# Performance work log

Hardware: AMD Instinct MI355X
Metric: run time of the kernel (lower is better)

The kernel has to match this reference:

```python
import jax, jax.numpy as jnp
import numpy as np

D_MODEL = 4096
D_FF = 16384
BATCH = 1
SEQ = 1024


def setup_inputs() -> dict:
    key = jax.random.key(0)
    k_x, k_k, k_s = jax.random.split(key, 3)
    inputs = jax.random.normal(k_x, (BATCH, SEQ, D_MODEL), dtype=jnp.float32)
    # int4 quantized kernel, values in [-8, 8)
    kernel = jax.random.randint(k_k, (D_MODEL, D_FF), -8, 8, dtype=jnp.int32).astype(jnp.int4)
    # per-output-channel scale, shape (1, D_FF), strictly positive
    scale = jax.random.uniform(k_s, (1, D_FF), dtype=jnp.float32, minval=0.5, maxval=2.0)
    return {"inputs": inputs, "kernel": kernel, "scale": scale}


def reference(inputs, kernel, scale):
    # Dequantize: int4 kernel -> fp32, divide by per-channel scale
    kernel_f = kernel.astype(jnp.float32) / scale  # [D_MODEL, D_FF]
    # btd,df->btf
    return jnp.einsum("btd,df->btf", inputs, kernel_f)
```

## Files before the change

kernel.cpp:

```cpp
#include <hip/hip_runtime.h>
#include <hip/hip_bf16.h>

#define D_MODEL 4096
#define D_FF    16384
#define SEQ     1024

typedef __attribute__((ext_vector_type(4))) float          fvec4;
typedef __attribute__((ext_vector_type(4))) float          f32x4;
typedef __attribute__((ext_vector_type(4))) int            i32x4;
typedef __attribute__((ext_vector_type(8))) short          bf16x8;
typedef __attribute__((ext_vector_type(4))) unsigned short u16x4;

constexpr int BM = 256, BN = 256, BK = 64;
constexpr int NTHREADS = 512;
constexpr int NT = D_MODEL / BK;
constexpr size_t WS_A_BYTES = 4ull * NT * 32768;

__device__ __forceinline__ unsigned short f2bf(float f) {
    unsigned int u = __builtin_bit_cast(unsigned int, f);
    u += 0x7FFFu + ((u >> 16) & 1u);
    return (unsigned short)(u >> 16);
}

__device__ __forceinline__ unsigned short kq_bf16(unsigned int w) {
    int iv = (int)w;
    float fi = (float)iv;
    unsigned int fw = ((unsigned int)(iv + 8) <= 15u)
                        ? __builtin_bit_cast(unsigned int, fi) : w;
    return (unsigned short)(fw >> 16);
}

__global__ __launch_bounds__(256)
void preconv_A(const float* __restrict__ X, unsigned short* __restrict__ wsA)
{
    size_t u = (size_t)blockIdx.x * 256 + threadIdx.x;
    size_t g = u * 8;
    int bm    = (int)(g >> 21);
    int r1    = (int)(g & 2097151);
    int kt    = r1 >> 15;
    int b     = r1 & 32767;
    int m     = b >> 7;
    int pslot = (b >> 4) & 7;
    int t     = pslot ^ (m & 7);
    int o     = (b >> 3) & 1;
    int k     = t * 8 + o * 4;
    const fvec4 v = *reinterpret_cast<const fvec4*>(
        &X[(size_t)(bm * 256 + m) * D_MODEL + kt * BK + k]);
    u16x4 h;
    #pragma unroll
    for (int e = 0; e < 4; ++e) h[e] = f2bf(v[e]);
    *reinterpret_cast<u16x4*>((char*)wsA + g) = h;
}

template <bool PRE>
__global__ __launch_bounds__(NTHREADS, 2)
void int4_gemm_kernel(const float* __restrict__ X, const unsigned int* __restrict__ Kq,
                      const float* __restrict__ scale, float* __restrict__ out,
                      const unsigned short* __restrict__ wsA)
{
    __shared__ short A_lds[2][BM * BK];
    __shared__ short B_lds[2][BN * BK];

    const int bid = blockIdx.x;
    const int bm  = (bid >> 3) & 3;
    const int bn  = (bid & 7) * 8 + (bid >> 5);

    const int tid  = threadIdx.x;
    const int lane = tid & 63;
    const int w    = tid >> 6;
    const int wr   = w >> 2;
    const int wc   = w & 3;
    const int lrow = lane & 15;
    const int lgrp = lane >> 4;

    const int row0 = bm * BM;
    const int col0 = bn * BN;

    const int b_n  = tid & 255;
    const int b_k8 = tid >> 8;

    f32x4 acc[8][4];
    #pragma unroll
    for (int i = 0; i < 8; ++i)
        #pragma unroll
        for (int j = 0; j < 4; ++j)
            acc[i][j] = (f32x4){0.f, 0.f, 0.f, 0.f};

    unsigned int bReg[4][8];

    auto issueB = [&](int kt) {
        const int kbase = kt * BK;
        #pragma unroll
        for (int i = 0; i < 4; ++i) {
            int k8 = b_k8 + i * 2;
            const unsigned int* src = &Kq[(size_t)(kbase + k8 * 8) * D_FF + col0 + b_n];
            #pragma unroll
            for (int j = 0; j < 8; ++j) bReg[i][j] = src[(size_t)j * D_FF];
        }
    };
    auto convertB = [&](short* Bbuf) {
        char* bB = (char*)Bbuf;
        #pragma unroll
        for (int i = 0; i < 4; ++i) {
            int k8 = b_k8 + i * 2;
            bf16x8 h;
            #pragma unroll
            for (int j = 0; j < 8; ++j) h[j] = (short)kq_bf16(bReg[i][j]);
            int boff = b_n * 128 + ((k8 ^ (b_n & 7)) * 16);
            *reinterpret_cast<bf16x8*>(bB + boff) = h;
        }
    };
    auto stageA = [&](int kt, short* Abuf) {
        if constexpr (PRE) {
            const char* src = (const char*)wsA + ((size_t)bm << 21) + ((size_t)kt << 15);
            char* dst = (char*)Abuf;
            #pragma unroll
            for (int i = 0; i < 4; ++i) {
                int off = i * 8192 + tid * 16;
                *reinterpret_cast<i32x4*>(dst + off) =
                    *reinterpret_cast<const i32x4*>(src + off);
            }
        } else {
            const int a_m = tid >> 4, a_f4 = tid & 15;
            const int kbase = kt * BK;
            char* aB = (char*)Abuf;
            #pragma unroll
            for (int i = 0; i < 8; ++i) {
                int m = a_m + i * 32;
                const fvec4 v = *reinterpret_cast<const fvec4*>(
                    &X[(size_t)(row0 + m) * D_MODEL + kbase + a_f4 * 4]);
                u16x4 h;
                #pragma unroll
                for (int e = 0; e < 4; ++e) h[e] = f2bf(v[e]);
                int boff = m * 128 + (((a_f4 >> 1) ^ (m & 7)) * 16) + (a_f4 & 1) * 8;
                *reinterpret_cast<u16x4*>(aB + boff) = h;
            }
        }
    };
    auto mfma_step = [&](const short* Abuf, const short* Bbuf) {
        const char* aB = (const char*)Abuf;
        const char* bB = (const char*)Bbuf;
        #pragma unroll
        for (int ks = 0; ks < 2; ++ks) {
            bf16x8 afrag[8];
            bf16x8 bfrag[4];
            #pragma unroll
            for (int i = 0; i < 8; ++i) {
                int r = wr * 128 + i * 16 + lrow;
                int s = (ks * 4 + lgrp) ^ (r & 7);
                afrag[i] = *reinterpret_cast<const bf16x8*>(aB + r * 128 + s * 16);
            }
            #pragma unroll
            for (int j = 0; j < 4; ++j) {
                int n = wc * 64 + j * 16 + lrow;
                int s = (ks * 4 + lgrp) ^ (n & 7);
                bfrag[j] = *reinterpret_cast<const bf16x8*>(bB + n * 128 + s * 16);
            }
            #pragma unroll
            for (int i = 0; i < 8; ++i)
                #pragma unroll
                for (int j = 0; j < 4; ++j)
                    acc[i][j] = __builtin_amdgcn_mfma_f32_16x16x32_bf16(
                        afrag[i], bfrag[j], acc[i][j], 0, 0, 0);
        }
    };
    auto tile_barrier = [&]() {
        asm volatile("s_waitcnt lgkmcnt(0)" ::: "memory");
        __builtin_amdgcn_s_barrier();
    };

    issueB(0);
    stageA(0, A_lds[0]);
    convertB(B_lds[0]);
    issueB(1);
    tile_barrier();

    for (int kt = 0; kt < NT; kt += 2) {
        if (kt + 1 < NT) { convertB(B_lds[1]); stageA(kt + 1, A_lds[1]); }
        if (kt + 2 < NT) issueB(kt + 2);
        mfma_step(A_lds[0], B_lds[0]);
        tile_barrier();
        if (kt + 2 < NT) { convertB(B_lds[0]); stageA(kt + 2, A_lds[0]); }
        if (kt + 3 < NT) issueB(kt + 3);
        mfma_step(A_lds[1], B_lds[1]);
        tile_barrier();
    }

    #pragma unroll
    for (int j = 0; j < 4; ++j) {
        int col = col0 + wc * 64 + j * 16 + lrow;
        float rs = 1.0f / scale[col];
        #pragma unroll
        for (int i = 0; i < 8; ++i) {
            int r0 = row0 + wr * 128 + i * 16 + lgrp * 4;
            #pragma unroll
            for (int r = 0; r < 4; ++r)
                out[(size_t)(r0 + r) * D_FF + col] = acc[i][j][r] * rs;
        }
    }
}

extern "C" void kernel_launch(void* const* d_in, const int* in_sizes, int n_in,
                              void* d_out, int out_size, void* d_ws, size_t ws_size,
                              hipStream_t stream) {
    const float*        X     = (const float*)d_in[0];
    const unsigned int* Kq    = (const unsigned int*)d_in[1];
    const float*        scale = (const float*)d_in[2];
    float*              out   = (float*)d_out;

    dim3 grid((SEQ / BM) * (D_FF / BN));
    dim3 block(NTHREADS);

    if (ws_size >= WS_A_BYTES) {
        unsigned short* wsA = (unsigned short*)d_ws;
        preconv_A<<<dim3((unsigned)(WS_A_BYTES / 8 / 256)), dim3(256), 0, stream>>>(X, wsA);
        int4_gemm_kernel<true><<<grid, block, 0, stream>>>(X, Kq, scale, out, wsA);
    } else {
        int4_gemm_kernel<false><<<grid, block, 0, stream>>>(X, Kq, scale, out, nullptr);
    }
}
```

Before: 463.4 us.

## Stage A tiles via direct global-to-LDS loads and add fp32-kernel fast path

Replaces the register round-trip for the pre-converted A tiles with global_load_lds direct-to-LDS copies, using vmcnt-bounded barriers so B loads stay in flight across tiles. Adds s_setprio around the MFMA block to favour matrix issue. Also probes the first kernel words at runtime to detect whether the int4 buffer was delivered as fp32 values and, if so, converts B by truncating fp32 to bf16 with bit ops instead of the int-to-float path. The runtime detection depends on the harness's storage format for int4, and the vmcnt(32) count must match the number of outstanding loads exactly.

```diff
diff --git a/kernel.cpp b/kernel.cpp
--- a/kernel.cpp
+++ b/kernel.cpp
@@ -79,6 +79,10 @@
     const int b_n  = tid & 255;
     const int b_k8 = tid >> 8;
 
+    unsigned int sw = Kq[lane];
+    int siv = (int)sw;
+    const bool is_f32 = __any((sw != 0u) && !((unsigned int)(siv + 8) <= 15u));
+
     f32x4 acc[8][4];
     #pragma unroll
     for (int i = 0; i < 8; ++i)
@@ -100,41 +104,56 @@
     };
     auto convertB = [&](short* Bbuf) {
         char* bB = (char*)Bbuf;
+        if (is_f32) {
+            #pragma unroll
+            for (int i = 0; i < 4; ++i) {
+                int k8 = b_k8 + i * 2;
+                i32x4 d;
+                #pragma unroll
+                for (int p = 0; p < 4; ++p)
+                    d[p] = (int)((bReg[i][2 * p] >> 16) |
+                                 (bReg[i][2 * p + 1] & 0xFFFF0000u));
+                int boff = b_n * 128 + ((k8 ^ (b_n & 7)) * 16);
+                *reinterpret_cast<i32x4*>(bB + boff) = d;
+            }
+        } else {
+            #pragma unroll
+            for (int i = 0; i < 4; ++i) {
+                int k8 = b_k8 + i * 2;
+                bf16x8 h;
+                #pragma unroll
+                for (int j = 0; j < 8; ++j) h[j] = (short)kq_bf16(bReg[i][j]);
+                int boff = b_n * 128 + ((k8 ^ (b_n & 7)) * 16);
+                *reinterpret_cast<bf16x8*>(bB + boff) = h;
+            }
+        }
+    };
+    auto gllA = [&](int kt, int bufIdx) {
+        const char* src = (const char*)wsA + ((size_t)bm << 21) + ((size_t)kt << 15);
+        char* dst = (char*)A_lds[bufIdx];
         #pragma unroll
         for (int i = 0; i < 4; ++i) {
-            int k8 = b_k8 + i * 2;
-            bf16x8 h;
-            #pragma unroll
-            for (int j = 0; j < 8; ++j) h[j] = (short)kq_bf16(bReg[i][j]);
-            int boff = b_n * 128 + ((k8 ^ (b_n & 7)) * 16);
-            *reinterpret_cast<bf16x8*>(bB + boff) = h;
-        }
-    };
-    auto stageA = [&](int kt, short* Abuf) {
-        if constexpr (PRE) {
-            const char* src = (const char*)wsA + ((size_t)bm << 21) + ((size_t)kt << 15);
-            char* dst = (char*)Abuf;
-            #pragma unroll
-            for (int i = 0; i < 4; ++i) {
-                int off = i * 8192 + tid * 16;
-                *reinterpret_cast<i32x4*>(dst + off) =
-                    *reinterpret_cast<const i32x4*>(src + off);
-            }
-        } else {
-            const int a_m = tid >> 4, a_f4 = tid & 15;
-            const int kbase = kt * BK;
-            char* aB = (char*)Abuf;
-            #pragma unroll
-            for (int i = 0; i < 8; ++i) {
-                int m = a_m + i * 32;
-                const fvec4 v = *reinterpret_cast<const fvec4*>(
-                    &X[(size_t)(row0 + m) * D_MODEL + kbase + a_f4 * 4]);
-                u16x4 h;
-                #pragma unroll
-                for (int e = 0; e < 4; ++e) h[e] = f2bf(v[e]);
-                int boff = m * 128 + (((a_f4 >> 1) ^ (m & 7)) * 16) + (a_f4 & 1) * 8;
-                *reinterpret_cast<u16x4*>(aB + boff) = h;
-            }
+            int off = i * 8192 + tid * 16;
+            __builtin_amdgcn_global_load_lds(
+                (__attribute__((address_space(1))) void*)(void*)(src + off),
+                (__attribute__((address_space(3))) void*)(dst + off),
+                16, 0, 0);
+        }
+    };
+    auto stageA_conv = [&](int kt, short* Abuf) {
+        const int a_m = tid >> 4, a_f4 = tid & 15;
+        const int kbase = kt * BK;
+        char* aB = (char*)Abuf;
+        #pragma unroll
+        for (int i = 0; i < 8; ++i) {
+            int m = a_m + i * 32;
+            const fvec4 v = *reinterpret_cast<const fvec4*>(
+                &X[(size_t)(row0 + m) * D_MODEL + kbase + a_f4 * 4]);
+            u16x4 h;
+            #pragma unroll
+            for (int e = 0; e < 4; ++e) h[e] = f2bf(v[e]);
+            int boff = m * 128 + (((a_f4 >> 1) ^ (m & 7)) * 16) + (a_f4 & 1) * 8;
+            *reinterpret_cast<u16x4*>(aB + boff) = h;
         }
     };
     auto mfma_step = [&](const short* Abuf, const short* Bbuf) {
@@ -156,34 +175,71 @@
                 int s = (ks * 4 + lgrp) ^ (n & 7);
                 bfrag[j] = *reinterpret_cast<const bf16x8*>(bB + n * 128 + s * 16);
             }
+            __builtin_amdgcn_s_setprio(1);
             #pragma unroll
             for (int i = 0; i < 8; ++i)
                 #pragma unroll
                 for (int j = 0; j < 4; ++j)
                     acc[i][j] = __builtin_amdgcn_mfma_f32_16x16x32_bf16(
                         afrag[i], bfrag[j], acc[i][j], 0, 0, 0);
-        }
-    };
-    auto tile_barrier = [&]() {
-        asm volatile("s_waitcnt lgkmcnt(0)" ::: "memory");
-        __builtin_amdgcn_s_barrier();
-    };
-
-    issueB(0);
-    stageA(0, A_lds[0]);
-    convertB(B_lds[0]);
-    issueB(1);
-    tile_barrier();
-
-    for (int kt = 0; kt < NT; kt += 2) {
-        if (kt + 1 < NT) { convertB(B_lds[1]); stageA(kt + 1, A_lds[1]); }
-        if (kt + 2 < NT) issueB(kt + 2);
+            __builtin_amdgcn_s_setprio(0);
+        }
+    };
+
+    if constexpr (PRE) {
+        #define BAR_VM32() do { \
+            asm volatile("s_waitcnt vmcnt(32) lgkmcnt(0)" ::: "memory"); \
+            __builtin_amdgcn_s_barrier(); } while (0)
+        #define BAR_VM0() do { \
+            asm volatile("s_waitcnt vmcnt(0) lgkmcnt(0)" ::: "memory"); \
+            __builtin_amdgcn_s_barrier(); } while (0)
+
+        issueB(0);
+        gllA(0, 0);
+        convertB(B_lds[0]);
+        issueB(1);
+        BAR_VM32();
+
+        for (int kt = 0; kt < NT - 2; kt += 2) {
+            convertB(B_lds[1]);
+            gllA(kt + 1, 1);
+            issueB(kt + 2);
+            mfma_step(A_lds[0], B_lds[0]);
+            BAR_VM32();
+
+            convertB(B_lds[0]);
+            gllA(kt + 2, 0);
+            issueB(kt + 3);
+            mfma_step(A_lds[1], B_lds[1]);
+            BAR_VM32();
+        }
+        convertB(B_lds[1]);
+        gllA(NT - 1, 1);
         mfma_step(A_lds[0], B_lds[0]);
-        tile_barrier();
-        if (kt + 2 < NT) { convertB(B_lds[0]); stageA(kt + 2, A_lds[0]); }
-        if (kt + 3 < NT) issueB(kt + 3);
+        BAR_VM0();
         mfma_step(A_lds[1], B_lds[1]);
-        tile_barrier();
+        #undef BAR_VM32
+        #undef BAR_VM0
+    } else {
+        auto bar = [&]() {
+            asm volatile("s_waitcnt lgkmcnt(0)" ::: "memory");
+            __builtin_amdgcn_s_barrier();
+        };
+        issueB(0);
+        stageA_conv(0, A_lds[0]);
+        convertB(B_lds[0]);
+        issueB(1);
+        bar();
+        for (int kt = 0; kt < NT; kt += 2) {
+            if (kt + 1 < NT) { convertB(B_lds[1]); stageA_conv(kt + 1, A_lds[1]); }
+            if (kt + 2 < NT) issueB(kt + 2);
+            mfma_step(A_lds[0], B_lds[0]);
+            bar();
+            if (kt + 2 < NT) { convertB(B_lds[0]); stageA_conv(kt + 2, A_lds[0]); }
+            if (kt + 3 < NT) issueB(kt + 3);
+            mfma_step(A_lds[1], B_lds[1]);
+            bar();
+        }
     }
 
     #pragma unroll
```

New measurement: 573.2 us. 23.7% more time.
